# Kernel tuning notes

Hardware: AMD Instinct MI355X
Metric: run time of the kernel (lower is better)

Reference implementation:

```python
import jax, jax.numpy as jnp
import numpy as np


def setup_inputs() -> dict:
    key = jax.random.key(0)
    k1, k2 = jax.random.split(key)
    N, DIM, K = 262144, 256, 256
    embeddings = jax.random.normal(k1, (N, DIM), dtype=jnp.float32)
    centroids = jax.random.normal(k2, (K, DIM), dtype=jnp.float32)  # faiss kmeans output
    return {"embeddings": embeddings, "centroids": centroids, "batch_id": 0}


def reference(embeddings, centroids, batch_id):
    # Batched equivalent of the per-query loop:
    #   for idx in range(N): dist = cdist(emb[idx:idx+1], centroids); top2 largest; take 2nd.
    x2 = jnp.sum(embeddings * embeddings, axis=1, keepdims=True)      # [N, 1]
    c2 = jnp.sum(centroids * centroids, axis=1)                       # [K]
    xc = jnp.einsum('nd,kd->nk', embeddings, centroids)               # [N, K]
    dist = jnp.sqrt(jnp.maximum(x2 + c2[None, :] - 2.0 * xc, 0.0))    # [N, K]
    # torch.topk defaults to largest=True; original takes indices[:, 1]
    _, top2_idx = jax.lax.top_k(dist, 2)                              # [N, 2]
    neg_embeddings = centroids[top2_idx[:, 1]]                        # [N, DIM]
    return neg_embeddings
```

## Files before the change

### kernel.cpp

```cpp
#include <hip/hip_runtime.h>
#include <hip/hip_bf16.h>


typedef __attribute__((ext_vector_type(8))) __bf16 bf16x8;
typedef __attribute__((ext_vector_type(4))) float f32x4;
typedef __attribute__((ext_vector_type(8))) unsigned short u16x8;

#define EPS 0.02f
#define CAP_MAX 65536
#define LROW 40

__device__ __forceinline__ void split_f32(float v, unsigned short& hi, unsigned short& lo) {
    unsigned u = __float_as_uint(v);
    hi = (unsigned short)(u >> 16);
    float hif = __uint_as_float(u & 0xFFFF0000u);
    float lov = v - hif;
    lo = (unsigned short)(__float_as_uint(lov) >> 16);
}

__device__ __forceinline__ unsigned f32_key(float s) {
    unsigned u = __float_as_uint(s);
    return u ^ ((unsigned)((int)u >> 31) | 0x80000000u);
}
__device__ __forceinline__ float key_to_float(unsigned key) {
    unsigned k = key & 0xFFFFFF00u;
    unsigned u = (k & 0x80000000u) ? (k ^ 0x80000000u) : ~k;
    return __uint_as_float(u);
}

__global__ __launch_bounds__(64) void cvt_kernel(const float* __restrict__ C,
    float* __restrict__ c2f, double* __restrict__ c2d,
    unsigned short* __restrict__ CHg, unsigned short* __restrict__ CLg) {
    const int k = blockIdx.x, l = threadIdx.x;
    float4 v = ((const float4*)(C + (size_t)k * 256))[l];
    unsigned short h0,h1,h2,h3, l0,l1,l2,l3;
    split_f32(v.x,h0,l0); split_f32(v.y,h1,l1); split_f32(v.z,h2,l2); split_f32(v.w,h3,l3);
    ((ushort4*)(CHg + (size_t)k * 256))[l] = make_ushort4(h0,h1,h2,h3);
    ((ushort4*)(CLg + (size_t)k * 256))[l] = make_ushort4(l0,l1,l2,l3);
    double s = (double)v.x*v.x + (double)v.y*v.y + (double)v.z*v.z + (double)v.w*v.w;
    #pragma unroll
    for (int off = 32; off >= 1; off >>= 1) s += __shfl_xor(s, off);
    if (l == 0) { c2f[k] = (float)s; c2d[k] = s; }
}

__global__ __launch_bounds__(256, 3) void score_kernel(
    const float* __restrict__ X, const unsigned short* __restrict__ CHg,
    const unsigned short* __restrict__ CLg, const float* __restrict__ C,
    const float* __restrict__ c2f, unsigned* __restrict__ counter,
    unsigned* __restrict__ list, unsigned cap, float* __restrict__ out) {

    __shared__ __align__(16) unsigned short SH[25600];
    __shared__ float c2s[256];
    __shared__ int bestIdx[64];

    unsigned short* XH  = SH;
    unsigned short* XL  = SH + 2560;
    unsigned short* CHl = SH + 5120;
    unsigned short* CLl = SH + 15360;

    const int t = threadIdx.x;
    const int rowBase = blockIdx.x * 64;
    c2s[t] = c2f[t];

    const int lane16 = t & 15, quad = (t >> 4) & 3, w = t >> 6;

    f32x4 acc[4][4];
    #pragma unroll
    for (int r = 0; r < 4; ++r)
        #pragma unroll
        for (int c = 0; c < 4; ++c) acc[r][c] = (f32x4)0.f;

    const int xr = t >> 2, xd = (t & 3) * 8;

    for (int chunk = 0; chunk < 8; ++chunk) {
        const int d0 = chunk * 32;
        const float4* gx = (const float4*)(X + (size_t)(rowBase + xr) * 256 + d0 + xd);
        float4 xa = gx[0], xb = gx[1];
        const u16x8* gh = (const u16x8*)(CHg + (size_t)t * 256 + d0);
        u16x8 ch0 = gh[0], ch1 = gh[1], ch2 = gh[2], ch3 = gh[3];
        const u16x8* gl = (const u16x8*)(CLg + (size_t)t * 256 + d0);
        u16x8 cl0 = gl[0], cl1 = gl[1], cl2 = gl[2], cl3 = gl[3];

        __syncthreads();
        {
            union { u16x8 v; unsigned short s[8]; } hu, lu;
            float xv[8] = {xa.x, xa.y, xa.z, xa.w, xb.x, xb.y, xb.z, xb.w};
            #pragma unroll
            for (int q = 0; q < 8; ++q) split_f32(xv[q], hu.s[q], lu.s[q]);
            *(u16x8*)(XH + xr * LROW + xd) = hu.v;
            *(u16x8*)(XL + xr * LROW + xd) = lu.v;
        }
        *(u16x8*)(CHl + t * LROW +  0) = ch0;
        *(u16x8*)(CHl + t * LROW +  8) = ch1;
        *(u16x8*)(CHl + t * LROW + 16) = ch2;
        *(u16x8*)(CHl + t * LROW + 24) = ch3;
        *(u16x8*)(CLl + t * LROW +  0) = cl0;
        *(u16x8*)(CLl + t * LROW +  8) = cl1;
        *(u16x8*)(CLl + t * LROW + 16) = cl2;
        *(u16x8*)(CLl + t * LROW + 24) = cl3;
        __syncthreads();

        bf16x8 ah[4], al[4];
        #pragma unroll
        for (int r = 0; r < 4; ++r) {
            ah[r] = *(const bf16x8*)(XH + (r * 16 + lane16) * LROW + quad * 8);
            al[r] = *(const bf16x8*)(XL + (r * 16 + lane16) * LROW + quad * 8);
        }
        #pragma unroll
        for (int c = 0; c < 4; ++c) {
            const int cb = (w * 64 + c * 16 + lane16) * LROW + quad * 8;
            bf16x8 bh = *(const bf16x8*)(CHl + cb);
            bf16x8 bl = *(const bf16x8*)(CLl + cb);
            #pragma unroll
            for (int r = 0; r < 4; ++r) {
                acc[r][c] = __builtin_amdgcn_mfma_f32_16x16x32_bf16(ah[r], bh, acc[r][c], 0, 0, 0);
                acc[r][c] = __builtin_amdgcn_mfma_f32_16x16x32_bf16(al[r], bh, acc[r][c], 0, 0, 0);
                acc[r][c] = __builtin_amdgcn_mfma_f32_16x16x32_bf16(ah[r], bl, acc[r][c], 0, 0, 0);
            }
        }
    }
    __syncthreads();

    unsigned* KEY = (unsigned*)SH;

    float cc2[4];
    #pragma unroll
    for (int c = 0; c < 4; ++c) cc2[c] = c2s[w * 64 + c * 16 + lane16];
    #pragma unroll
    for (int r = 0; r < 4; ++r) {
        #pragma unroll
        for (int i = 0; i < 4; ++i) {
            const int row = r * 16 + quad * 4 + i;
            unsigned k1 = 0, k2 = 0, k3 = 0;
            #pragma unroll
            for (int c = 0; c < 4; ++c) {
                float s = cc2[c] - 2.f * acc[r][c][i];
                unsigned cent = (unsigned)(w * 64 + c * 16 + lane16);
                unsigned key = (f32_key(s) & 0xFFFFFF00u) | (255u - cent);
                if (key > k1)      { k3 = k2; k2 = k1; k1 = key; }
                else if (key > k2) { k3 = k2; k2 = key; }
                else if (key > k3) { k3 = key; }
            }
            const int base = row * 192 + (w * 16 + lane16) * 3;
            KEY[base] = k1; KEY[base + 1] = k2; KEY[base + 2] = k3;
        }
    }
    __syncthreads();

    {
        const int row = t & 63, qr = t >> 6;
        const int base = row * 192 + qr * 48;
        unsigned k1 = 0, k2 = 0, k3 = 0;
        for (int q = 0; q < 48; ++q) {
            unsigned key = KEY[base + q];
            if (key > k1)      { k3 = k2; k2 = k1; k1 = key; }
            else if (key > k2) { k3 = k2; k2 = key; }
            else if (key > k3) { k3 = key; }
        }
        KEY[base] = k1; KEY[base + 1] = k2; KEY[base + 2] = k3;
    }
    __syncthreads();

    if (t < 64) {
        unsigned k1 = 0, k2 = 0, k3 = 0;
        #pragma unroll
        for (int qr = 0; qr < 4; ++qr) {
            const int base = t * 192 + qr * 48;
            #pragma unroll
            for (int q = 0; q < 3; ++q) {
                unsigned key = KEY[base + q];
                if (key > k1)      { k3 = k2; k2 = k1; k1 = key; }
                else if (key > k2) { k3 = k2; k2 = key; }
                else if (key > k3) { k3 = key; }
            }
        }
        bestIdx[t] = 255 - (int)(k2 & 0xFFu);
        float s1 = key_to_float(k1), s2 = key_to_float(k2), s3 = key_to_float(k3);
        if (s1 - s2 < EPS || s2 - s3 < EPS) {
            unsigned p = atomicAdd(counter, 1u);
            if (p < cap) list[p] = (unsigned)(rowBase + t);
        }
    }
    __syncthreads();

    {
        const int r = t >> 2, q0 = t & 3;
        const int c = bestIdx[r];
        const float4* src = (const float4*)(C + (size_t)c * 256);
        float4* dst = (float4*)(out + (size_t)(rowBase + r) * 256);
        #pragma unroll
        for (int q = 0; q < 16; ++q) dst[q0 + 4 * q] = src[q0 + 4 * q];
    }
}

__global__ __launch_bounds__(256) void refine_kernel(
    const float* __restrict__ X, const float* __restrict__ C,
    const double* __restrict__ c2d, const unsigned* __restrict__ counter,
    const unsigned* __restrict__ list, unsigned cap, float* __restrict__ out) {

    __shared__ float xs[256];
    __shared__ double sh[256];
    __shared__ int b2s;
    unsigned count = *counter;
    if (count > cap) count = cap;
    const int k = threadIdx.x;

    for (unsigned idx = blockIdx.x; idx < count; idx += gridDim.x) {
        const unsigned row = list[idx];
        xs[k] = X[(size_t)row * 256 + k];
        __syncthreads();
        const float4* cp = (const float4*)(C + (size_t)k * 256);
        double a = 0.0;
        #pragma unroll 4
        for (int j = 0; j < 64; ++j) {
            float4 c4 = cp[j];
            a += (double)c4.x * xs[4 * j + 0] + (double)c4.y * xs[4 * j + 1]
               + (double)c4.z * xs[4 * j + 2] + (double)c4.w * xs[4 * j + 3];
        }
        sh[k] = c2d[k] - 2.0 * a;
        __syncthreads();
        if (k == 0) {
            double b1 = -1e300, b2 = -1e300;
            int i1 = 0, i2 = 0;
            for (int q = 0; q < 256; ++q) {
                double s = sh[q];
                if (s > b1)      { b2 = b1; i2 = i1; b1 = s; i1 = q; }
                else if (s > b2) { b2 = s;  i2 = q; }
            }
            b2s = i2;
        }
        __syncthreads();
        const int csel = b2s;
        if (k < 64) {
            const float4* src = (const float4*)(C + (size_t)csel * 256);
            float4* dst = (float4*)(out + (size_t)row * 256);
            dst[k] = src[k];
        }
        __syncthreads();
    }
}

extern "C" void kernel_launch(void* const* d_in, const int* in_sizes, int n_in,
                              void* d_out, int out_size, void* d_ws, size_t ws_size,
                              hipStream_t stream) {
    const float* X = (const float*)d_in[0];
    const float* C = (const float*)d_in[1];
    float* out = (float*)d_out;
    const int N = in_sizes[0] / 256;

    unsigned* counter = (unsigned*)d_ws;
    float* c2f = (float*)((char*)d_ws + 64);
    double* c2d = (double*)((char*)d_ws + 2048);
    unsigned short* CHg = (unsigned short*)((char*)d_ws + 4096);
    unsigned short* CLg = (unsigned short*)((char*)d_ws + 135168);
    unsigned* list = (unsigned*)((char*)d_ws + 266240);
    unsigned cap = 0;
    if (ws_size > 266240) {
        size_t c = (ws_size - 266240) / 4;
        cap = (unsigned)(c < (size_t)CAP_MAX ? c : (size_t)CAP_MAX);
    }

    hipMemsetAsync(d_ws, 0, 64, stream);
    cvt_kernel<<<256, 64, 0, stream>>>(C, c2f, c2d, CHg, CLg);
    score_kernel<<<N / 64, 256, 0, stream>>>(X, CHg, CLg, C, c2f, counter, list, cap, out);
    refine_kernel<<<1024, 256, 0, stream>>>(X, C, c2d, counter, list, cap, out);
}
```

Measured before the change: 626.7 us.

## Pre-tile centroid splits, load via global_load_lds, prefetch X, shuffle-based top3

The cvt kernel now writes the centroid hi/lo bf16 halves in an MFMA-fragment-tiled layout, so the score kernel can copy them straight into LDS with global_load_lds and then read them with contiguous per-lane loads instead of padded rows. X for the next chunk is prefetched into registers while the current chunk computes. The per-row top-3 reduction uses cross-lane shuffles instead of two LDS passes and a barrier, which also shrinks LDS use. The cost is extra index arithmetic and a tight coupling between the global layout and the MFMA operand layout.

```diff
diff --git a/kernel.cpp b/kernel.cpp
--- a/kernel.cpp
+++ b/kernel.cpp
@@ -8,7 +8,6 @@
 
 #define EPS 0.02f
 #define CAP_MAX 65536
-#define LROW 40
 
 __device__ __forceinline__ void split_f32(float v, unsigned short& hi, unsigned short& lo) {
     unsigned u = __float_as_uint(v);
@@ -26,6 +25,18 @@
     unsigned k = key & 0xFFFFFF00u;
     unsigned u = (k & 0x80000000u) ? (k ^ 0x80000000u) : ~k;
     return __uint_as_float(u);
+}
+
+__device__ __forceinline__ void ins3(unsigned& k1, unsigned& k2, unsigned& k3, unsigned v) {
+    if (v > k1)      { k3 = k2; k2 = k1; k1 = v; }
+    else if (v > k2) { k3 = k2; k2 = v; }
+    else if (v > k3) { k3 = v; }
+}
+
+__device__ __forceinline__ void gload16(const unsigned short* g, unsigned short* l) {
+    __builtin_amdgcn_global_load_lds(
+        (const __attribute__((address_space(1))) void*)g,
+        (__attribute__((address_space(3))) void*)l, 16, 0, 0);
 }
 
 __global__ __launch_bounds__(64) void cvt_kernel(const float* __restrict__ C,
@@ -35,11 +46,16 @@
     float4 v = ((const float4*)(C + (size_t)k * 256))[l];
     unsigned short h0,h1,h2,h3, l0,l1,l2,l3;
     split_f32(v.x,h0,l0); split_f32(v.y,h1,l1); split_f32(v.z,h2,l2); split_f32(v.w,h3,l3);
-    ((ushort4*)(CHg + (size_t)k * 256))[l] = make_ushort4(h0,h1,h2,h3);
-    ((ushort4*)(CLg + (size_t)k * 256))[l] = make_ushort4(l0,l1,l2,l3);
+    const int d = l * 4;
+    const size_t off = (size_t)(d >> 5) * 8192
+                     + (size_t)(k >> 4) * 512
+                     + (size_t)((((d >> 3) & 3) << 4) | (k & 15)) * 8
+                     + (d & 7);
+    *(ushort4*)(CHg + off) = make_ushort4(h0,h1,h2,h3);
+    *(ushort4*)(CLg + off) = make_ushort4(l0,l1,l2,l3);
     double s = (double)v.x*v.x + (double)v.y*v.y + (double)v.z*v.z + (double)v.w*v.w;
     #pragma unroll
-    for (int off = 32; off >= 1; off >>= 1) s += __shfl_xor(s, off);
+    for (int off2 = 32; off2 >= 1; off2 >>= 1) s += __shfl_xor(s, off2);
     if (l == 0) { c2f[k] = (float)s; c2d[k] = s; }
 }
 
@@ -49,20 +65,21 @@
     const float* __restrict__ c2f, unsigned* __restrict__ counter,
     unsigned* __restrict__ list, unsigned cap, float* __restrict__ out) {
 
-    __shared__ __align__(16) unsigned short SH[25600];
+    __shared__ __align__(16) unsigned short SH[20480];
     __shared__ float c2s[256];
     __shared__ int bestIdx[64];
 
-    unsigned short* XH  = SH;
-    unsigned short* XL  = SH + 2560;
-    unsigned short* CHl = SH + 5120;
-    unsigned short* CLl = SH + 15360;
+    unsigned short* XH2 = SH;
+    unsigned short* XL2 = SH + 2048;
+    unsigned short* CH2 = SH + 4096;
+    unsigned short* CL2 = SH + 12288;
 
     const int t = threadIdx.x;
     const int rowBase = blockIdx.x * 64;
     c2s[t] = c2f[t];
 
-    const int lane16 = t & 15, quad = (t >> 4) & 3, w = t >> 6;
+    const int lane = t & 63, w = t >> 6;
+    const int lane16 = t & 15, quad = (t >> 4) & 3;
 
     f32x4 acc[4][4];
     #pragma unroll
@@ -70,47 +87,53 @@
         #pragma unroll
         for (int c = 0; c < 4; ++c) acc[r][c] = (f32x4)0.f;
 
-    const int xr = t >> 2, xd = (t & 3) * 8;
+    const int xr = t >> 2, xs = t & 3;
+    const float* xbase = X + (size_t)(rowBase + xr) * 256 + xs * 8;
+    const int xoff = (xr >> 4) * 512 + ((xs << 4) | (xr & 15)) * 8;
+
+    float4 xa = ((const float4*)xbase)[0];
+    float4 xb = ((const float4*)xbase)[1];
 
     for (int chunk = 0; chunk < 8; ++chunk) {
-        const int d0 = chunk * 32;
-        const float4* gx = (const float4*)(X + (size_t)(rowBase + xr) * 256 + d0 + xd);
-        float4 xa = gx[0], xb = gx[1];
-        const u16x8* gh = (const u16x8*)(CHg + (size_t)t * 256 + d0);
-        u16x8 ch0 = gh[0], ch1 = gh[1], ch2 = gh[2], ch3 = gh[3];
-        const u16x8* gl = (const u16x8*)(CLg + (size_t)t * 256 + d0);
-        u16x8 cl0 = gl[0], cl1 = gl[1], cl2 = gl[2], cl3 = gl[3];
-
-        __syncthreads();
+        union { u16x8 v; unsigned short s[8]; } hu, lu;
         {
-            union { u16x8 v; unsigned short s[8]; } hu, lu;
             float xv[8] = {xa.x, xa.y, xa.z, xa.w, xb.x, xb.y, xb.z, xb.w};
             #pragma unroll
             for (int q = 0; q < 8; ++q) split_f32(xv[q], hu.s[q], lu.s[q]);
-            *(u16x8*)(XH + xr * LROW + xd) = hu.v;
-            *(u16x8*)(XL + xr * LROW + xd) = lu.v;
-        }
-        *(u16x8*)(CHl + t * LROW +  0) = ch0;
-        *(u16x8*)(CHl + t * LROW +  8) = ch1;
-        *(u16x8*)(CHl + t * LROW + 16) = ch2;
-        *(u16x8*)(CHl + t * LROW + 24) = ch3;
-        *(u16x8*)(CLl + t * LROW +  0) = cl0;
-        *(u16x8*)(CLl + t * LROW +  8) = cl1;
-        *(u16x8*)(CLl + t * LROW + 16) = cl2;
-        *(u16x8*)(CLl + t * LROW + 24) = cl3;
-        __syncthreads();
+        }
+
+        __syncthreads();
+
+        {
+            const size_t gb = (size_t)chunk * 8192 + (size_t)(w * 4) * 512 + (size_t)lane * 8;
+            const int lb = (w * 4) * 512 + lane * 8;
+            #pragma unroll
+            for (int s2 = 0; s2 < 4; ++s2) {
+                gload16(CHg + gb + s2 * 512, CH2 + lb + s2 * 512);
+                gload16(CLg + gb + s2 * 512, CL2 + lb + s2 * 512);
+            }
+        }
+        *(u16x8*)(XH2 + xoff) = hu.v;
+        *(u16x8*)(XL2 + xoff) = lu.v;
+        __syncthreads();
+
+        if (chunk < 7) {
+            const float* nx = xbase + (chunk + 1) * 32;
+            xa = ((const float4*)nx)[0];
+            xb = ((const float4*)nx)[1];
+        }
 
         bf16x8 ah[4], al[4];
         #pragma unroll
         for (int r = 0; r < 4; ++r) {
-            ah[r] = *(const bf16x8*)(XH + (r * 16 + lane16) * LROW + quad * 8);
-            al[r] = *(const bf16x8*)(XL + (r * 16 + lane16) * LROW + quad * 8);
+            ah[r] = *(const bf16x8*)(XH2 + r * 512 + lane * 8);
+            al[r] = *(const bf16x8*)(XL2 + r * 512 + lane * 8);
         }
         #pragma unroll
         for (int c = 0; c < 4; ++c) {
-            const int cb = (w * 64 + c * 16 + lane16) * LROW + quad * 8;
-            bf16x8 bh = *(const bf16x8*)(CHl + cb);
-            bf16x8 bl = *(const bf16x8*)(CLl + cb);
+            const int cb = (w * 4 + c) * 512 + lane * 8;
+            bf16x8 bh = *(const bf16x8*)(CH2 + cb);
+            bf16x8 bl = *(const bf16x8*)(CL2 + cb);
             #pragma unroll
             for (int r = 0; r < 4; ++r) {
                 acc[r][c] = __builtin_amdgcn_mfma_f32_16x16x32_bf16(ah[r], bh, acc[r][c], 0, 0, 0);
@@ -121,58 +144,46 @@
     }
     __syncthreads();
 
-    unsigned* KEY = (unsigned*)SH;
+    unsigned* WKEY = (unsigned*)SH;
 
     float cc2[4];
     #pragma unroll
     for (int c = 0; c < 4; ++c) cc2[c] = c2s[w * 64 + c * 16 + lane16];
+
     #pragma unroll
     for (int r = 0; r < 4; ++r) {
         #pragma unroll
         for (int i = 0; i < 4; ++i) {
-            const int row = r * 16 + quad * 4 + i;
             unsigned k1 = 0, k2 = 0, k3 = 0;
             #pragma unroll
             for (int c = 0; c < 4; ++c) {
                 float s = cc2[c] - 2.f * acc[r][c][i];
                 unsigned cent = (unsigned)(w * 64 + c * 16 + lane16);
                 unsigned key = (f32_key(s) & 0xFFFFFF00u) | (255u - cent);
-                if (key > k1)      { k3 = k2; k2 = k1; k1 = key; }
-                else if (key > k2) { k3 = k2; k2 = key; }
-                else if (key > k3) { k3 = key; }
-            }
-            const int base = row * 192 + (w * 16 + lane16) * 3;
-            KEY[base] = k1; KEY[base + 1] = k2; KEY[base + 2] = k3;
-        }
-    }
-    __syncthreads();
-
-    {
-        const int row = t & 63, qr = t >> 6;
-        const int base = row * 192 + qr * 48;
-        unsigned k1 = 0, k2 = 0, k3 = 0;
-        for (int q = 0; q < 48; ++q) {
-            unsigned key = KEY[base + q];
-            if (key > k1)      { k3 = k2; k2 = k1; k1 = key; }
-            else if (key > k2) { k3 = k2; k2 = key; }
-            else if (key > k3) { k3 = key; }
-        }
-        KEY[base] = k1; KEY[base + 1] = k2; KEY[base + 2] = k3;
+                ins3(k1, k2, k3, key);
+            }
+            #pragma unroll
+            for (int m = 1; m <= 8; m <<= 1) {
+                unsigned o1 = __shfl_xor(k1, m);
+                unsigned o2 = __shfl_xor(k2, m);
+                unsigned o3 = __shfl_xor(k3, m);
+                ins3(k1, k2, k3, o1); ins3(k1, k2, k3, o2); ins3(k1, k2, k3, o3);
+            }
+            if (lane16 == 0) {
+                const int row = r * 16 + quad * 4 + i;
+                unsigned* p = WKEY + row * 13 + w * 3;
+                p[0] = k1; p[1] = k2; p[2] = k3;
+            }
+        }
     }
     __syncthreads();
 
     if (t < 64) {
         unsigned k1 = 0, k2 = 0, k3 = 0;
         #pragma unroll
-        for (int qr = 0; qr < 4; ++qr) {
-            const int base = t * 192 + qr * 48;
-            #pragma unroll
-            for (int q = 0; q < 3; ++q) {
-                unsigned key = KEY[base + q];
-                if (key > k1)      { k3 = k2; k2 = k1; k1 = key; }
-                else if (key > k2) { k3 = k2; k2 = key; }
-                else if (key > k3) { k3 = key; }
-            }
+        for (int w2 = 0; w2 < 4; ++w2) {
+            const unsigned* p = WKEY + t * 13 + w2 * 3;
+            ins3(k1, k2, k3, p[0]); ins3(k1, k2, k3, p[1]); ins3(k1, k2, k3, p[2]);
         }
         bestIdx[t] = 255 - (int)(k2 & 0xFFu);
         float s1 = key_to_float(k1), s2 = key_to_float(k2), s3 = key_to_float(k3);
```

Result: slower. 1.096 ms (+74.9%).
